# Optimization experiments

Hardware: AMD Instinct MI355X
Metric: run time of the kernel (lower is better)

Reference implementation:

```python
import jax, jax.numpy as jnp
import numpy as np
import math

B, L, D, H = 2, 1024, 1024, 16
DK = D // H  # 64
R = 130      # 2k+2 relative-position buckets (k=64)


def setup_inputs() -> dict:
    key = jax.random.key(0)
    ks = jax.random.split(key, 16)
    s = 1.0 / math.sqrt(D)
    return {
        "hidden_state": jax.random.normal(ks[0], (B, L, D), jnp.float32),
        "rel_q": jax.random.normal(ks[1], (1, H, R, DK), jnp.float32),
        "rel_k": jax.random.normal(ks[2], (1, H, R, DK), jnp.float32),
        "Wq": jax.random.normal(ks[3], (D, D), jnp.float32) * s,
        "bq": jnp.zeros((D,), jnp.float32),
        "Wk": jax.random.normal(ks[4], (D, D), jnp.float32) * s,
        "bk": jnp.zeros((D,), jnp.float32),
        "Wv": jax.random.normal(ks[5], (D, D), jnp.float32) * s,
        "bv": jnp.zeros((D,), jnp.float32),
        "Wo": jax.random.normal(ks[6], (D, D), jnp.float32) * s,
        "bo": jnp.zeros((D,), jnp.float32),
        "pos_indices": jax.random.randint(ks[7], (B, H, L, L), 0, R, jnp.int64 if jax.config.jax_enable_x64 else jnp.int32),
        "mask": jax.random.bernoulli(ks[8], 0.1, (B, 1, 1, L)),
    }


def reference(hidden_state, rel_q, rel_k, Wq, bq, Wk, bk, Wv, bv, Wo, bo, pos_indices, mask):
    # projections (torch Linear: x @ W.T + b), split into heads -> [B,H,L,DK]
    def proj(x, W, b):
        return (x @ W.T + b).reshape(B, L, H, DK).transpose(0, 2, 1, 3)

    q = proj(hidden_state, Wq, bq)
    k = proj(hidden_state, Wk, bk)
    v = proj(hidden_state, Wv, bv)

    scale = 1.0 / math.sqrt(DK * 3)  # scale_factor = 3 (c2c + p2c + c2p)

    # content-to-content: [B,H,L,L]
    c2c = jnp.einsum("bhid,bhjd->bhij", q, k) * scale

    # position-to-content: rel_q @ k.T -> [B,H,R,L], gather rows by pos_indices
    p2c = jnp.einsum("hrd,bhjd->bhrj", rel_q[0] * scale, k)
    p2c = jnp.take_along_axis(p2c, pos_indices, axis=-2)  # [B,H,L,L]

    # content-to-position: q @ rel_k.T -> [B,H,L,R], gather cols by pos_indices.T
    c2p = jnp.einsum("bhid,hrd->bhir", q, rel_k[0]) * scale
    c2p = jnp.take_along_axis(c2p, jnp.swapaxes(pos_indices, -2, -1), axis=-1)  # [B,H,L,L]

    scores = c2c + p2c + c2p
    scores = jnp.where(mask, jnp.float32(-1e9), scores)
    probs = jax.nn.softmax(scores, axis=-1)  # dropout p=0.0 (eval)

    ctx = jnp.einsum("bhij,bhjd->bhid", probs, v)
    out = ctx.transpose(0, 2, 1, 3).reshape(B, L, D) @ Wo.T + bo
    return out
```

## Files before the change

### kernel.cpp

```cpp
#include <hip/hip_runtime.h>
#include <hip/hip_fp16.h>

typedef _Float16 f16;
typedef f16 f16x8 __attribute__((ext_vector_type(8)));
typedef f16 f16x4 __attribute__((ext_vector_type(4)));
typedef f16 f16x2 __attribute__((ext_vector_type(2)));
typedef float f32x4 __attribute__((ext_vector_type(4)));

#define DEVI static __device__ __forceinline__

constexpr int Bc = 2, Lc = 1024, Dc = 1024, Hc = 16, DKc = 64, Rc = 130;
constexpr float SCALE = 0.07216878364870323f;
constexpr float MASKV = -30000.0f;

DEVI uint2 pack8(int4 a, int4 b) {
    unsigned lo = (unsigned)(a.x & 255) | ((unsigned)(a.y & 255) << 8) |
                  ((unsigned)(a.z & 255) << 16) | ((unsigned)(a.w & 255) << 24);
    unsigned hi = (unsigned)(b.x & 255) | ((unsigned)(b.y & 255) << 8) |
                  ((unsigned)(b.z & 255) << 16) | ((unsigned)(b.w & 255) << 24);
    return make_uint2(lo, hi);
}

DEVI int i4get(const int4& v, int u) {
    return u == 0 ? v.x : (u == 1 ? v.y : (u == 2 ? v.z : v.w));
}

DEVI int packf16(float a, float b) {
    f16x2 t = {(f16)a, (f16)b};
    return __builtin_bit_cast(int, t);
}

__global__ __launch_bounds__(256) void gemm_qkv(const float* __restrict__ A,
                                                const float* __restrict__ wq,
                                                const float* __restrict__ wk,
                                                const float* __restrict__ wv,
                                                const float* __restrict__ bq,
                                                const float* __restrict__ bk,
                                                const float* __restrict__ bv,
                                                f16* __restrict__ qw,
                                                f16* __restrict__ kw,
                                                f16* __restrict__ vtw) {
    constexpr int K = 1024;
    __shared__ __align__(16) f16 As[128][40];
    __shared__ __align__(16) f16 Bs[64][40];
    const int tid = threadIdx.x, lane = tid & 63, w = tid >> 6;
    const int wm = w >> 1, wn = w & 1;
    const int m0 = blockIdx.y * 128, n0 = blockIdx.x * 64;
    const int which = n0 >> 10;
    const float* __restrict__ W = which == 0 ? wq : (which == 1 ? wk : wv);
    const int n0L = n0 & 1023;

    f32x4 acc[4][2];
#pragma unroll
    for (int i = 0; i < 4; ++i)
#pragma unroll
        for (int j = 0; j < 2; ++j) acc[i][j] = (f32x4){0.f, 0.f, 0.f, 0.f};

    for (int k0 = 0; k0 < K; k0 += 32) {
#pragma unroll
        for (int rep = 0; rep < 4; ++rep) {
            int id = tid + rep * 256;
            int row = id >> 3, c = (id & 7) * 4;
            float4 v = *(const float4*)&A[(size_t)(m0 + row) * K + k0 + c];
            *(f16x4*)&As[row][c] = (f16x4){(f16)v.x, (f16)v.y, (f16)v.z, (f16)v.w};
        }
#pragma unroll
        for (int rep = 0; rep < 2; ++rep) {
            int id = tid + rep * 256;
            int row = id >> 3, c = (id & 7) * 4;
            float4 v = *(const float4*)&W[(size_t)(n0L + row) * K + k0 + c];
            *(f16x4*)&Bs[row][c] = (f16x4){(f16)v.x, (f16)v.y, (f16)v.z, (f16)v.w};
        }
        __syncthreads();
        f16x8 a[4], bb[2];
#pragma unroll
        for (int mf = 0; mf < 4; ++mf)
            a[mf] = *(const f16x8*)&As[wm * 64 + mf * 16 + (lane & 15)][(lane >> 4) * 8];
#pragma unroll
        for (int nf = 0; nf < 2; ++nf)
            bb[nf] = *(const f16x8*)&Bs[wn * 32 + nf * 16 + (lane & 15)][(lane >> 4) * 8];
#pragma unroll
        for (int mf = 0; mf < 4; ++mf)
#pragma unroll
            for (int nf = 0; nf < 2; ++nf)
                acc[mf][nf] = __builtin_amdgcn_mfma_f32_16x16x32_f16(a[mf], bb[nf], acc[mf][nf], 0, 0, 0);
        __syncthreads();
    }

    const float* bp = which == 0 ? bq : (which == 1 ? bk : bv);
    const float scl = which == 0 ? SCALE : 1.0f;
#pragma unroll
    for (int mf = 0; mf < 4; ++mf)
#pragma unroll
        for (int nf = 0; nf < 2; ++nf) {
            int rowb = m0 + wm * 64 + mf * 16 + (lane >> 4) * 4;
            int col = n0 + wn * 32 + nf * 16 + (lane & 15);
            int colL = col & 1023;
            int h = colL >> 6, d = colL & 63;
            float bv_ = bp[colL];
            if (which == 2) {
                int b = rowb >> 10, i = rowb & (Lc - 1);
                f16x4 pk = {(f16)(acc[mf][nf][0] + bv_), (f16)(acc[mf][nf][1] + bv_),
                            (f16)(acc[mf][nf][2] + bv_), (f16)(acc[mf][nf][3] + bv_)};
                *(f16x4*)&vtw[(((size_t)(b * Hc + h)) * DKc + d) * Lc + i] = pk;
            } else {
                f16* dst = which ? kw : qw;
#pragma unroll
                for (int rg = 0; rg < 4; ++rg) {
                    int row = rowb + rg;
                    int b = row >> 10, i = row & (Lc - 1);
                    dst[(((size_t)(b * Hc + h)) * Lc + i) * DKc + d] =
                        (f16)((acc[mf][nf][rg] + bv_) * scl);
                }
            }
        }
}

__global__ __launch_bounds__(256) void rel_mfma(const f16* __restrict__ rowmat,
                                                const float* __restrict__ relmat,
                                                f16* __restrict__ outT, float scl) {
    __shared__ __align__(16) f16 As[144][72];
    __shared__ __align__(16) f16 Bs[64][72];
    const int tid = threadIdx.x, lane = tid & 63, w = tid >> 6;
    const int bh = blockIdx.y, h = bh & (Hc - 1);
    const int i0 = blockIdx.x * 64;
    const size_t bhR = (size_t)bh * Rc;

    for (int e = tid; e < Rc * 16; e += 256) {
        int r = e >> 4, c = (e & 15) * 4;
        float4 v = *(const float4*)&relmat[((size_t)h * Rc + r) * DKc + c];
        *(f16x4*)&As[r][c] = (f16x4){(f16)v.x, (f16)v.y, (f16)v.z, (f16)v.w};
    }
    if (tid < 224) {
        int r = 130 + (tid >> 4), c = (tid & 15) * 4;
        *(f16x4*)&As[r][c] = (f16x4){(f16)0.f, (f16)0.f, (f16)0.f, (f16)0.f};
    }
    for (int e = tid; e < 64 * 8; e += 256) {
        int i = e >> 3, c = (e & 7) * 8;
        *(f16x8*)&Bs[i][c] = *(const f16x8*)&rowmat[((size_t)bh * Lc + i0 + i) * DKc + c];
    }
    __syncthreads();

    f16x8 bfr[2];
#pragma unroll
    for (int ks = 0; ks < 2; ++ks)
        bfr[ks] = *(const f16x8*)&Bs[w * 16 + (lane & 15)][ks * 32 + (lane >> 4) * 8];
    f32x4 acc[9];
#pragma unroll
    for (int m = 0; m < 9; ++m) acc[m] = (f32x4){0.f, 0.f, 0.f, 0.f};
#pragma unroll
    for (int m = 0; m < 9; ++m)
#pragma unroll
        for (int ks = 0; ks < 2; ++ks) {
            f16x8 af = *(const f16x8*)&As[m * 16 + (lane & 15)][ks * 32 + (lane >> 4) * 8];
            acc[m] = __builtin_amdgcn_mfma_f32_16x16x32_f16(af, bfr[ks], acc[m], 0, 0, 0);
        }
#pragma unroll
    for (int m = 0; m < 9; ++m)
#pragma unroll
        for (int rg = 0; rg < 4; ++rg) {
            int r = m * 16 + (lane >> 4) * 4 + rg;
            if (r < Rc)
                outT[(bhR + r) * Lc + i0 + w * 16 + (lane & 15)] = (f16)(acc[m][rg] * scl);
        }
}

__global__ __launch_bounds__(512) void attn_v9(const f16* __restrict__ q,
                                               const f16* __restrict__ k,
                                               const f16* __restrict__ vt,
                                               const f16* __restrict__ p2c,
                                               const f16* __restrict__ c2pT,
                                               const int* __restrict__ pos,
                                               const int* __restrict__ mask,
                                               f16* __restrict__ opart,
                                               float2* __restrict__ mlpart) {
    __shared__ f16 tc2p[Rc][132];
    __shared__ f16 tp2c[2][Rc][36];
    __shared__ __align__(16) f16 Ks[2][32][72];
    __shared__ __align__(16) f16 Vs[2][64][40];
    __shared__ unsigned char pJI[2][32][136];
    __shared__ float madd[2][32];

    const int tid = threadIdx.x, lane = tid & 63, w = tid >> 6;
    const int flat = blockIdx.x;
    const int ib = flat >> 6;
    const int sp = (flat >> 5) & 1;
    const int bh = flat & 31;
    const int b = bh >> 4, h = bh & 15;
    const int i0 = ib * 128;
    const int j0base = sp * 512;
    const size_t bhL = (size_t)bh * Lc;
    const size_t bhR = (size_t)bh * Rc;
    f16* __restrict__ op = opart + (size_t)sp * Bc * Lc * Dc;
    float2* __restrict__ mlp = mlpart + (size_t)sp * Bc * Hc * Lc;
    const int g = lane >> 4, il16 = lane & 15, irow = w * 16 + il16;

    for (int e = tid; e < Rc * 32; e += 512) {
        int r = e >> 5, c4 = (e & 31) * 4;
        *(f16x4*)&tc2p[r][c4] = *(const f16x4*)&c2pT[(bhR + r) * Lc + i0 + c4];
    }

    f16x8 qa[2];
    {
        const f16* qp = &q[(bhL + i0 + irow) * DKc + g * 8];
        qa[0] = *(const f16x8*)qp;
        qa[1] = *(const f16x8*)(qp + 32);
    }

    float mrun = -1e30f, lrun = 0.f;
    f32x4 oacc[4];
#pragma unroll
    for (int df = 0; df < 4; ++df) oacc[df] = (f32x4){0.f, 0.f, 0.f, 0.f};

    f16x4 kreg, vreg;
    int4 prA0, prA1, prB0, prB1;
    f16x4 tpr0, tpr1, tpr2;
    uint2 pjreg;
    float mreg;

#define FV_ISSUE(J0X)                                                                        \
    {                                                                                        \
        kreg = *(const f16x4*)&k[(bhL + (J0X) + (tid >> 4)) * DKc + (tid & 15) * 4];         \
        vreg = *(const f16x4*)&vt[((size_t)bh * DKc + (tid >> 3)) * Lc + (J0X) + (tid & 7) * 4]; \
        {                                                                                    \
            int e_ = tid;                                                                    \
            tpr0 = *(const f16x4*)&p2c[(bhR + (e_ >> 3)) * Lc + (J0X) + (e_ & 7) * 4];       \
            e_ = tid + 512;                                                                  \
            tpr1 = *(const f16x4*)&p2c[(bhR + (e_ >> 3)) * Lc + (J0X) + (e_ & 7) * 4];       \
            if (tid < 16) {                                                                  \
                e_ = tid + 1024;                                                             \
                tpr2 = *(const f16x4*)&p2c[(bhR + (e_ >> 3)) * Lc + (J0X) + (e_ & 7) * 4];   \
            }                                                                                \
        }                                                                                    \
        {                                                                                    \
            const int* pp = &pos[(bhL + (J0X) + (tid >> 4)) * Lc + i0 + (tid & 15) * 8];     \
            pjreg = pack8(*(const int4*)pp, *(const int4*)(pp + 4));                         \
        }                                                                                    \
        if (tid < 32) mreg = mask[b * Lc + (J0X) + tid] ? MASKV : 0.f;                       \
        {                                                                                    \
            const int* prow = &pos[(bhL + i0 + irow) * Lc + (J0X) + g * 4];                  \
            prB0 = *(const int4*)prow;                                                       \
            prB1 = *(const int4*)(prow + 16);                                                \
        }                                                                                    \
    }

#define FV_COMMIT(NB)                                                                        \
    {                                                                                        \
        *(f16x4*)&Ks[NB][tid >> 4][(tid & 15) * 4] = kreg;                                   \
        *(f16x4*)&Vs[NB][tid >> 3][(tid & 7) * 4] = vreg;                                    \
        int e_ = tid;                                                                        \
        *(f16x4*)&tp2c[NB][e_ >> 3][(e_ & 7) * 4] = tpr0;                                    \
        e_ = tid + 512;                                                                      \
        *(f16x4*)&tp2c[NB][e_ >> 3][(e_ & 7) * 4] = tpr1;                                    \
        if (tid < 16) { e_ = tid + 1024; *(f16x4*)&tp2c[NB][e_ >> 3][(e_ & 7) * 4] = tpr2; } \
        *(uint2*)&pJI[NB][tid >> 4][(tid & 15) * 8] = pjreg;                                 \
        if (tid < 32) madd[NB][tid] = mreg;                                                  \
    }

    FV_ISSUE(j0base);
    FV_COMMIT(0);
    prA0 = prB0; prA1 = prB1;
    __syncthreads();

    for (int t = 0; t < 16; ++t) {
        const int cur = t & 1;
        const int j0 = j0base + t * 32;
        if (t < 15) FV_ISSUE(j0 + 32);

        f32x4 s[2];
        s[0] = (f32x4){0.f, 0.f, 0.f, 0.f};
        s[1] = (f32x4){0.f, 0.f, 0.f, 0.f};
#pragma unroll
        for (int jf = 0; jf < 2; ++jf)
#pragma unroll
            for (int ks = 0; ks < 2; ++ks) {
                f16x8 kb = *(const f16x8*)&Ks[cur][jf * 16 + il16][ks * 32 + g * 8];
                s[jf] = __builtin_amdgcn_mfma_f32_16x16x32_f16(kb, qa[ks], s[jf], 0, 0, 0);
            }

        float sv[8];
#pragma unroll
        for (int u = 0; u < 8; ++u) {
            int jcol = (u < 4) ? (g * 4 + u) : (16 + g * 4 + (u - 4));
            int r1 = (u < 4) ? i4get(prA0, u) : i4get(prA1, u - 4);
            int r2 = pJI[cur][jcol][irow];
            sv[u] = s[u >> 2][u & 3] + (float)tp2c[cur][r1][jcol] +
                    (float)tc2p[r2][irow] + madd[cur][jcol];
        }

        float tm = sv[0];
#pragma unroll
        for (int e = 1; e < 8; ++e) tm = fmaxf(tm, sv[e]);
        tm = fmaxf(tm, __shfl_xor(tm, 16));
        tm = fmaxf(tm, __shfl_xor(tm, 32));
        float mnew = fmaxf(mrun, tm);
        float alpha = __expf(mrun - mnew);
        float rs = 0.f;
#pragma unroll
        for (int e = 0; e < 8; ++e) {
            sv[e] = __expf(sv[e] - mnew);
            rs += sv[e];
        }
        rs += __shfl_xor(rs, 16);
        rs += __shfl_xor(rs, 32);
        lrun = lrun * alpha + rs;
        mrun = mnew;

        int lo0 = packf16(sv[0], sv[1]), lo1 = packf16(sv[2], sv[3]);
        int hi0 = packf16(sv[4], sv[5]), hi1 = packf16(sv[6], sv[7]);
        int s0 = ((g & 1) << 5) | il16, s1 = s0 + 16;
        int a0 = __shfl(lo0, s0), a1 = __shfl(lo1, s0);
        int a2 = __shfl(lo0, s1), a3 = __shfl(lo1, s1);
        int b0 = __shfl(hi0, s0), b1 = __shfl(hi1, s0);
        int b2 = __shfl(hi0, s1), b3 = __shfl(hi1, s1);
        int4 paw = (g < 2) ? make_int4(a0, a1, a2, a3) : make_int4(b0, b1, b2, b3);
        f16x8 pa = __builtin_bit_cast(f16x8, paw);

        float al[4];
#pragma unroll
        for (int rg = 0; rg < 4; ++rg)
            al[rg] = __shfl(alpha, (lane & 48) | (g * 4 + rg));
#pragma unroll
        for (int df = 0; df < 4; ++df)
#pragma unroll
            for (int rg = 0; rg < 4; ++rg) oacc[df][rg] *= al[rg];

#pragma unroll
        for (int df = 0; df < 4; ++df) {
            f16x8 vb = *(const f16x8*)&Vs[cur][df * 16 + il16][g * 8];
            oacc[df] = __builtin_amdgcn_mfma_f32_16x16x32_f16(pa, vb, oacc[df], 0, 0, 0);
        }

        if (t < 15) {
            FV_COMMIT(cur ^ 1);
            prA0 = prB0; prA1 = prB1;
        }
        __syncthreads();
    }

#pragma unroll
    for (int df = 0; df < 4; ++df)
#pragma unroll
        for (int rg = 0; rg < 4; ++rg) {
            int i = i0 + w * 16 + g * 4 + rg;
            int d = df * 16 + il16;
            op[((size_t)(b * Lc + i) * Hc + h) * DKc + d] = (f16)oacc[df][rg];
        }
    if (g == 0) mlp[bhL + i0 + irow] = make_float2(mrun, lrun);
#undef FV_ISSUE
#undef FV_COMMIT
}

__global__ __launch_bounds__(256) void merge_ns(const f16* __restrict__ op,
                                                const float2* __restrict__ ml,
                                                f16* __restrict__ ctx, int ns) {
    int t4 = blockIdx.x * 256 + threadIdx.x;
    int t = t4 * 4;
    int b = t >> 20;
    int rem = t & 1048575;
    int i = rem >> 10;
    int h = (rem & 1023) >> 6;
    int row = ((b << 4) + h) * Lc + i;
    const size_t On = (size_t)Bc * Lc * Dc, Mn = (size_t)Bc * Hc * Lc;
    float mx = -1e30f;
    for (int s = 0; s < ns; ++s) mx = fmaxf(mx, ml[s * Mn + row].x);
    float l = 0.f;
    float v[4] = {0.f, 0.f, 0.f, 0.f};
    for (int s = 0; s < ns; ++s) {
        float2 m = ml[s * Mn + row];
        float w_ = __expf(m.x - mx);
        l += m.y * w_;
        f16x4 o = *(const f16x4*)&op[s * On + t];
#pragma unroll
        for (int e = 0; e < 4; ++e) v[e] += (float)o[e] * w_;
    }
    float rl = 1.0f / l;
    f16x4 r = {(f16)(v[0] * rl), (f16)(v[1] * rl), (f16)(v[2] * rl), (f16)(v[3] * rl)};
    *(f16x4*)&ctx[t] = r;
}

__global__ __launch_bounds__(256) void gemm_out(const f16* __restrict__ A,
                                                const float* __restrict__ W,
                                                const float* __restrict__ bias,
                                                float* __restrict__ outf) {
    constexpr int K = 1024;
    __shared__ __align__(16) f16 As[128][40];
    __shared__ __align__(16) f16 Bs[64][40];
    const int tid = threadIdx.x, lane = tid & 63, w = tid >> 6;
    const int wm = w >> 1, wn = w & 1;
    const int m0 = blockIdx.y * 128, n0 = blockIdx.x * 64;

    f32x4 acc[4][2];
#pragma unroll
    for (int i = 0; i < 4; ++i)
#pragma unroll
        for (int j = 0; j < 2; ++j) acc[i][j] = (f32x4){0.f, 0.f, 0.f, 0.f};

    for (int k0 = 0; k0 < K; k0 += 32) {
#pragma unroll
        for (int rep = 0; rep < 2; ++rep) {
            int id = tid + rep * 256;
            int row = id >> 2, c = (id & 3) * 8;
            *(f16x8*)&As[row][c] = *(const f16x8*)&A[(size_t)(m0 + row) * K + k0 + c];
        }
#pragma unroll
        for (int rep = 0; rep < 2; ++rep) {
            int id = tid + rep * 256;
            int row = id >> 3, c = (id & 7) * 4;
            float4 v = *(const float4*)&W[(size_t)(n0 + row) * K + k0 + c];
            *(f16x4*)&Bs[row][c] = (f16x4){(f16)v.x, (f16)v.y, (f16)v.z, (f16)v.w};
        }
        __syncthreads();
        f16x8 a[4], bb[2];
#pragma unroll
        for (int mf = 0; mf < 4; ++mf)
            a[mf] = *(const f16x8*)&As[wm * 64 + mf * 16 + (lane & 15)][(lane >> 4) * 8];
#pragma unroll
        for (int nf = 0; nf < 2; ++nf)
            bb[nf] = *(const f16x8*)&Bs[wn * 32 + nf * 16 + (lane & 15)][(lane >> 4) * 8];
#pragma unroll
        for (int mf = 0; mf < 4; ++mf)
#pragma unroll
            for (int nf = 0; nf < 2; ++nf)
                acc[mf][nf] = __builtin_amdgcn_mfma_f32_16x16x32_f16(a[mf], bb[nf], acc[mf][nf], 0, 0, 0);
        __syncthreads();
    }
#pragma unroll
    for (int mf = 0; mf < 4; ++mf)
#pragma unroll
        for (int nf = 0; nf < 2; ++nf) {
            int rowb = m0 + wm * 64 + mf * 16 + (lane >> 4) * 4;
            int col = n0 + wn * 32 + nf * 16 + (lane & 15);
            float bv = bias[col];
#pragma unroll
            for (int rg = 0; rg < 4; ++rg)
                outf[(size_t)(rowb + rg) * Dc + col] = acc[mf][nf][rg] + bv;
        }
}

extern "C" void kernel_launch(void* const* d_in, const int* in_sizes, int n_in,
                              void* d_out, int out_size, void* d_ws, size_t ws_size,
                              hipStream_t stream) {
    const float* hid = (const float*)d_in[0];
    const float* rel_q = (const float*)d_in[1];
    const float* rel_k = (const float*)d_in[2];
    const float* Wq = (const float*)d_in[3];
    const float* bq = (const float*)d_in[4];
    const float* Wk = (const float*)d_in[5];
    const float* bk = (const float*)d_in[6];
    const float* Wv = (const float*)d_in[7];
    const float* bv = (const float*)d_in[8];
    const float* Wo = (const float*)d_in[9];
    const float* bo = (const float*)d_in[10];
    const int* pos = (const int*)d_in[11];
    const int* mask = (const int*)d_in[12];

    const size_t MiB = 1ull << 20;
    const size_t tblBytes = (size_t)Bc * Hc * Rc * Lc * 2;
    const size_t opBytes = (size_t)Bc * Lc * Dc * 2;
    const size_t mlBytes = (size_t)Bc * Hc * Lc * 8;
    const size_t need = (12 + 18 + 13) * MiB + 65536;
    if (need > ws_size) return;

    char* ws = (char*)d_ws;
    size_t off = 0;
    auto alloc = [&](size_t bytes) {
        void* p = ws + off;
        off += (bytes + 255) & ~(size_t)255;
        return p;
    };

    f16* qw = (f16*)alloc(opBytes);
    f16* kw = (f16*)alloc(opBytes);
    f16* vtw = (f16*)alloc(opBytes);
    f16* c2pTw = (f16*)alloc(tblBytes);
    f16* p2cw = (f16*)alloc(tblBytes);
    char* u = (char*)alloc(13 * MiB);
    f16* oparts = (f16*)u;
    float2* mls = (float2*)(u + 2 * opBytes);
    f16* ctxh = (f16*)(u + 2 * (opBytes + mlBytes));

    gemm_qkv<<<dim3(48, 16), 256, 0, stream>>>(hid, Wq, Wk, Wv, bq, bk, bv, qw, kw, vtw);
    rel_mfma<<<dim3(16, 32), 256, 0, stream>>>(qw, rel_k, c2pTw, 1.0f);
    rel_mfma<<<dim3(16, 32), 256, 0, stream>>>(kw, rel_q, p2cw, SCALE);
    attn_v9<<<512, 512, 0, stream>>>(qw, kw, vtw, p2cw, c2pTw, pos, mask, oparts, mls);
    merge_ns<<<2048, 256, 0, stream>>>(oparts, mls, ctxh, 2);
    gemm_out<<<dim3(16, 16), 256, 0, stream>>>(ctxh, Wo, bo, (float*)d_out);
}
```

Baseline: 131.2 us.

## Fold key mask into p2c table, skip redundant rescale, prioritize MFMA waves

The key-padding mask is added into the p2c relative table during rel_mfma, since every p2c entry for key column j carries the mask of j. This removes the per-tile mask load, the shared-memory array and one add per score in the attention kernel. The online-softmax rescale of the accumulator now runs only when some lane's running max grows, and s_setprio raises wave priority around the MFMA blocks. Adding -30000 into an fp16 table sits close to the fp16 limit and costs some precision on masked entries, and the __any branch adds a wave-uniform divergence check.

```diff
diff --git a/kernel.cpp b/kernel.cpp
--- a/kernel.cpp
+++ b/kernel.cpp
@@ -118,7 +118,8 @@
 
 __global__ __launch_bounds__(256) void rel_mfma(const f16* __restrict__ rowmat,
                                                 const float* __restrict__ relmat,
-                                                f16* __restrict__ outT, float scl) {
+                                                f16* __restrict__ outT, float scl,
+                                                const int* __restrict__ mask) {
     __shared__ __align__(16) f16 As[144][72];
     __shared__ __align__(16) f16 Bs[64][72];
     const int tid = threadIdx.x, lane = tid & 63, w = tid >> 6;
@@ -141,6 +142,10 @@
     }
     __syncthreads();
 
+    const int ocol = i0 + w * 16 + (lane & 15);
+    float ma = 0.f;
+    if (mask) ma = mask[(bh >> 4) * Lc + ocol] ? MASKV : 0.f;
+
     f16x8 bfr[2];
 #pragma unroll
     for (int ks = 0; ks < 2; ++ks)
@@ -161,25 +166,23 @@
         for (int rg = 0; rg < 4; ++rg) {
             int r = m * 16 + (lane >> 4) * 4 + rg;
             if (r < Rc)
-                outT[(bhR + r) * Lc + i0 + w * 16 + (lane & 15)] = (f16)(acc[m][rg] * scl);
-        }
-}
-
-__global__ __launch_bounds__(512) void attn_v9(const f16* __restrict__ q,
-                                               const f16* __restrict__ k,
-                                               const f16* __restrict__ vt,
-                                               const f16* __restrict__ p2c,
-                                               const f16* __restrict__ c2pT,
-                                               const int* __restrict__ pos,
-                                               const int* __restrict__ mask,
-                                               f16* __restrict__ opart,
-                                               float2* __restrict__ mlpart) {
+                outT[(bhR + r) * Lc + ocol] = (f16)(acc[m][rg] * scl + ma);
+        }
+}
+
+__global__ __launch_bounds__(512) void attn_v10(const f16* __restrict__ q,
+                                                const f16* __restrict__ k,
+                                                const f16* __restrict__ vt,
+                                                const f16* __restrict__ p2c,
+                                                const f16* __restrict__ c2pT,
+                                                const int* __restrict__ pos,
+                                                f16* __restrict__ opart,
+                                                float2* __restrict__ mlpart) {
     __shared__ f16 tc2p[Rc][132];
     __shared__ f16 tp2c[2][Rc][36];
     __shared__ __align__(16) f16 Ks[2][32][72];
     __shared__ __align__(16) f16 Vs[2][64][40];
     __shared__ unsigned char pJI[2][32][136];
-    __shared__ float madd[2][32];
 
     const int tid = threadIdx.x, lane = tid & 63, w = tid >> 6;
     const int flat = blockIdx.x;
@@ -216,7 +219,6 @@
     int4 prA0, prA1, prB0, prB1;
     f16x4 tpr0, tpr1, tpr2;
     uint2 pjreg;
-    float mreg;
 
 #define FV_ISSUE(J0X)                                                                        \
     {                                                                                        \
@@ -236,7 +238,6 @@
             const int* pp = &pos[(bhL + (J0X) + (tid >> 4)) * Lc + i0 + (tid & 15) * 8];     \
             pjreg = pack8(*(const int4*)pp, *(const int4*)(pp + 4));                         \
         }                                                                                    \
-        if (tid < 32) mreg = mask[b * Lc + (J0X) + tid] ? MASKV : 0.f;                       \
         {                                                                                    \
             const int* prow = &pos[(bhL + i0 + irow) * Lc + (J0X) + g * 4];                  \
             prB0 = *(const int4*)prow;                                                       \
@@ -254,7 +255,6 @@
         *(f16x4*)&tp2c[NB][e_ >> 3][(e_ & 7) * 4] = tpr1;                                    \
         if (tid < 16) { e_ = tid + 1024; *(f16x4*)&tp2c[NB][e_ >> 3][(e_ & 7) * 4] = tpr2; } \
         *(uint2*)&pJI[NB][tid >> 4][(tid & 15) * 8] = pjreg;                                 \
-        if (tid < 32) madd[NB][tid] = mreg;                                                  \
     }
 
     FV_ISSUE(j0base);
@@ -270,6 +270,7 @@
         f32x4 s[2];
         s[0] = (f32x4){0.f, 0.f, 0.f, 0.f};
         s[1] = (f32x4){0.f, 0.f, 0.f, 0.f};
+        __builtin_amdgcn_s_setprio(1);
 #pragma unroll
         for (int jf = 0; jf < 2; ++jf)
 #pragma unroll
@@ -277,6 +278,7 @@
                 f16x8 kb = *(const f16x8*)&Ks[cur][jf * 16 + il16][ks * 32 + g * 8];
                 s[jf] = __builtin_amdgcn_mfma_f32_16x16x32_f16(kb, qa[ks], s[jf], 0, 0, 0);
             }
+        __builtin_amdgcn_s_setprio(0);
 
         float sv[8];
 #pragma unroll
@@ -284,8 +286,7 @@
             int jcol = (u < 4) ? (g * 4 + u) : (16 + g * 4 + (u - 4));
             int r1 = (u < 4) ? i4get(prA0, u) : i4get(prA1, u - 4);
             int r2 = pJI[cur][jcol][irow];
-            sv[u] = s[u >> 2][u & 3] + (float)tp2c[cur][r1][jcol] +
-                    (float)tc2p[r2][irow] + madd[cur][jcol];
+            sv[u] = s[u >> 2][u & 3] + (float)tp2c[cur][r1][jcol] + (float)tc2p[r2][irow];
         }
 
         float tm = sv[0];
@@ -293,18 +294,29 @@
         for (int e = 1; e < 8; ++e) tm = fmaxf(tm, sv[e]);
         tm = fmaxf(tm, __shfl_xor(tm, 16));
         tm = fmaxf(tm, __shfl_xor(tm, 32));
-        float mnew = fmaxf(mrun, tm);
-        float alpha = __expf(mrun - mnew);
+        if (__any(tm > mrun)) {
+            float mnew = fmaxf(mrun, tm);
+            float alpha = __expf(mrun - mnew);
+            mrun = mnew;
+            lrun *= alpha;
+            float al[4];
+#pragma unroll
+            for (int rg = 0; rg < 4; ++rg)
+                al[rg] = __shfl(alpha, (lane & 48) | (g * 4 + rg));
+#pragma unroll
+            for (int df = 0; df < 4; ++df)
+#pragma unroll
+                for (int rg = 0; rg < 4; ++rg) oacc[df][rg] *= al[rg];
+        }
         float rs = 0.f;
 #pragma unroll
         for (int e = 0; e < 8; ++e) {
-            sv[e] = __expf(sv[e] - mnew);
+            sv[e] = __expf(sv[e] - mrun);
             rs += sv[e];
         }
         rs += __shfl_xor(rs, 16);
         rs += __shfl_xor(rs, 32);
-        lrun = lrun * alpha + rs;
-        mrun = mnew;
+        lrun += rs;
 
         int lo0 = packf16(sv[0], sv[1]), lo1 = packf16(sv[2], sv[3]);
         int hi0 = packf16(sv[4], sv[5]), hi1 = packf16(sv[6], sv[7]);
@@ -316,20 +328,13 @@
         int4 paw = (g < 2) ? make_int4(a0, a1, a2, a3) : make_int4(b0, b1, b2, b3);
         f16x8 pa = __builtin_bit_cast(f16x8, paw);
 
-        float al[4];
-#pragma unroll
-        for (int rg = 0; rg < 4; ++rg)
-            al[rg] = __shfl(alpha, (lane & 48) | (g * 4 + rg));
-#pragma unroll
-        for (int df = 0; df < 4; ++df)
-#pragma unroll
-            for (int rg = 0; rg < 4; ++rg) oacc[df][rg] *= al[rg];
-
+        __builtin_amdgcn_s_setprio(1);
 #pragma unroll
         for (int df = 0; df < 4; ++df) {
             f16x8 vb = *(const f16x8*)&Vs[cur][df * 16 + il16][g * 8];
             oacc[df] = __builtin_amdgcn_mfma_f32_16x16x32_f16(pa, vb, oacc[df], 0, 0, 0);
         }
+        __builtin_amdgcn_s_setprio(0);
 
         if (t < 15) {
             FV_COMMIT(cur ^ 1);
@@ -481,9 +486,9 @@
     f16* ctxh = (f16*)(u + 2 * (opBytes + mlBytes));
 
     gemm_qkv<<<dim3(48, 16), 256, 0, stream>>>(hid, Wq, Wk, Wv, bq, bk, bv, qw, kw, vtw);
-    rel_mfma<<<dim3(16, 32), 256, 0, stream>>>(qw, rel_k, c2pTw, 1.0f);
-    rel_mfma<<<dim3(16, 32), 256, 0, stream>>>(kw, rel_q, p2cw, SCALE);
-    attn_v9<<<512, 512, 0, stream>>>(qw, kw, vtw, p2cw, c2pTw, pos, mask, oparts, mls);
+    rel_mfma<<<dim3(16, 32), 256, 0, stream>>>(qw, rel_k, c2pTw, 1.0f, nullptr);
+    rel_mfma<<<dim3(16, 32), 256, 0, stream>>>(kw, rel_q, p2cw, SCALE, mask);
+    attn_v10<<<512, 512, 0, stream>>>(qw, kw, vtw, p2cw, c2pTw, pos, oparts, mls);
     merge_ns<<<2048, 256, 0, stream>>>(oparts, mls, ctxh, 2);
     gemm_out<<<dim3(16, 16), 256, 0, stream>>>(ctxh, Wo, bo, (float*)d_out);
 }
```

New measurement: 130.4 us, median of 2. No clear change (-0.6%).
